# Performance work log

Hardware: AMD Instinct MI355X
Metric: run time of the kernel (lower is better)

The kernel has to match this reference:

```python
import jax, jax.numpy as jnp
import numpy as np

N_NODES = 50000
N_EDGES = 800000
IN_C = 64
OUT_C = 64
HEADS = 4
N_LAYERS = 2
BN_EPS = 1e-5
NEG_SLOPE = 0.2


def setup_inputs() -> dict:
    key = jax.random.key(0)
    ks = jax.random.split(key, 20)
    inp = {
        "x": jax.random.normal(ks[0], (N_NODES, IN_C), dtype=jnp.float32),
        "edge_index": jax.random.randint(ks[1], (2, N_EDGES), 0, N_NODES, dtype=jnp.int64),
        "edge_weight": jax.random.uniform(ks[2], (N_EDGES,), dtype=jnp.float32),
    }
    # per-layer GATConv + BN params (glorot-ish init)
    for i in range(N_LAYERS):
        k = 3 + i * 5
        scale = 1.0 / np.sqrt(IN_C)
        inp[f"W{i}"] = jax.random.normal(ks[k], (IN_C, HEADS * OUT_C), dtype=jnp.float32) * scale
        inp[f"asrc{i}"] = jax.random.normal(ks[k + 1], (HEADS, OUT_C), dtype=jnp.float32) * scale
        inp[f"adst{i}"] = jax.random.normal(ks[k + 2], (HEADS, OUT_C), dtype=jnp.float32) * scale
        inp[f"b{i}"] = jnp.zeros((OUT_C,), dtype=jnp.float32)
        inp[f"gamma{i}"] = jnp.ones((OUT_C,), dtype=jnp.float32)
        inp[f"beta{i}"] = jnp.zeros((OUT_C,), dtype=jnp.float32)
    return inp


def _gat_layer(x, src, dst, W, a_src, a_dst, b):
    # x: [N, C_in]; src/dst: [E'] (with self loops). Per-head dim = OUT_C.
    xh = (x @ W).reshape(-1, HEADS, OUT_C)          # [N, H, C]
    al_src = jnp.sum(xh * a_src[None], axis=-1)      # [N, H]
    al_dst = jnp.sum(xh * a_dst[None], axis=-1)      # [N, H]
    e = jax.nn.leaky_relu(al_src[src] + al_dst[dst], NEG_SLOPE)  # [E', H]
    # segment softmax over edges sharing a destination node
    m = jax.lax.stop_gradient(jax.ops.segment_max(e, dst, num_segments=N_NODES))
    p = jnp.exp(e - m[dst])
    denom = jax.ops.segment_sum(p, dst, num_segments=N_NODES)
    alpha = p / (denom[dst] + 1e-16)                 # [E', H]
    out = jax.ops.segment_sum(alpha[:, :, None] * xh[src], dst, num_segments=N_NODES)  # [N,H,C]
    return out.mean(axis=1) + b                      # concat=False -> mean over heads


def _batchnorm(x, gamma, beta):
    mu = x.mean(axis=0)
    var = x.var(axis=0)
    return gamma * (x - mu) * jax.lax.rsqrt(var + BN_EPS) + beta


def reference(x, edge_index, edge_weight, W0, asrc0, adst0, b0, gamma0, beta0,
              W1, asrc1, adst1, b1, gamma1, beta1):
    # edge_weight is passed as edge_attr to PyG GATConv but edge_dim=None -> ignored.
    loop = jnp.arange(N_NODES, dtype=edge_index.dtype)
    src = jnp.concatenate([edge_index[0], loop])  # add_self_loops=True (PyG default)
    dst = jnp.concatenate([edge_index[1], loop])
    params = [(W0, asrc0, adst0, b0, gamma0, beta0),
              (W1, asrc1, adst1, b1, gamma1, beta1)]
    saved = None
    for (W, a_s, a_d, b, g, bt) in params:
        x = _gat_layer(x, src, dst, W, a_s, a_d, b)
        saved = x
        x = _batchnorm(x, g, bt)
        x = jax.nn.relu(x)
        # dropout(0.5) is identity in eval mode
    return (x, saved)
```

## Files before the change

kernel.cpp:

```cpp
#include <hip/hip_runtime.h>
#include <stdint.h>

#define NEG_SLOPE 0.2f
#define BN_EPS 1e-5f

typedef __attribute__((ext_vector_type(8))) short bf16x8;
typedef __attribute__((ext_vector_type(4))) float f32x4;

__device__ __forceinline__ float bf2f(unsigned short u) {
  union { unsigned int i; float f; } v; v.i = ((unsigned int)u) << 16; return v.f;
}
__device__ __forceinline__ float asf(unsigned int u) {
  union { unsigned int i; float f; } v; v.i = u; return v.f;
}
__device__ __forceinline__ unsigned short f2bf(float f) {
  union { float f; unsigned int i; } v; v.f = f;
  unsigned int i = v.i;
  return (unsigned short)((i + 0x7fffu + ((i >> 16) & 1u)) >> 16);
}
__device__ __forceinline__ float loadF(const void* p, long long i, int f32) {
  return f32 ? ((const float*)p)[i] : bf2f(((const unsigned short*)p)[i]);
}
__device__ __forceinline__ int edge_at(const void* ei, long long idx, int is64) {
  return is64 ? (int)((const long long*)ei)[idx] : ((const int*)ei)[idx];
}

__global__ void detect_kernel(const unsigned short* __restrict__ x,
                              const int* __restrict__ ei32,
                              int* __restrict__ flags) {
  __shared__ int wild, oddnz;
  if (threadIdx.x == 0) { wild = 0; oddnz = 0; }
  __syncthreads();
  int lw = 0, lo = 0;
  for (int i = threadIdx.x; i < 4096; i += 256) {
    unsigned short u = x[i];
    int ex = (u >> 7) & 0xFF;
    if (ex >= 0x86) lw++;
    if (ei32[2 * i + 1] != 0) lo++;
  }
  if (lw) atomicAdd(&wild, lw);
  if (lo) atomicAdd(&oddnz, lo);
  __syncthreads();
  if (threadIdx.x == 0) { flags[0] = (wild > 64) ? 1 : 0; flags[1] = (oddnz == 0) ? 1 : 0; }
}

__global__ __launch_bounds__(256) void wtrans_kernel(
    const void* __restrict__ W0, const void* __restrict__ as0, const void* __restrict__ ad0,
    const void* __restrict__ W1, const void* __restrict__ as1, const void* __restrict__ ad1,
    const int* __restrict__ flags,
    unsigned short* __restrict__ WTx0, unsigned short* __restrict__ WTx1) {
  const void* W = blockIdx.x ? W1 : W0;
  const void* asrc = blockIdx.x ? as1 : as0;
  const void* adst = blockIdx.x ? ad1 : ad0;
  unsigned short* WTx = blockIdx.x ? WTx1 : WTx0;
  int f32 = flags[0];
  __shared__ unsigned short Wl[64 * 258];
  int t = threadIdx.x;
  for (int i = t; i < 64 * 256; i += 256) {
    int k = i >> 8, c = i & 255;
    Wl[k * 258 + c] = f32 ? f2bf(((const float*)W)[i]) : ((const unsigned short*)W)[i];
  }
  __syncthreads();
  {
    int c = t;
    #pragma unroll
    for (int k8 = 0; k8 < 64; k8 += 8) {
      unsigned int p0 = (unsigned int)Wl[(k8 + 0) * 258 + c] | ((unsigned int)Wl[(k8 + 1) * 258 + c] << 16);
      unsigned int p1 = (unsigned int)Wl[(k8 + 2) * 258 + c] | ((unsigned int)Wl[(k8 + 3) * 258 + c] << 16);
      unsigned int p2 = (unsigned int)Wl[(k8 + 4) * 258 + c] | ((unsigned int)Wl[(k8 + 5) * 258 + c] << 16);
      unsigned int p3 = (unsigned int)Wl[(k8 + 6) * 258 + c] | ((unsigned int)Wl[(k8 + 7) * 258 + c] << 16);
      uint4 pk; pk.x = p0; pk.y = p1; pk.z = p2; pk.w = p3;
      *(uint4*)&WTx[c * 64 + k8] = pk;
    }
  }
  for (int idx = t; idx < 512; idx += 256) {
    int r = idx >> 6;
    int k = idx & 63;
    int h = r & 3;
    const void* av = (r >> 2) ? adst : asrc;
    float acc = 0.f;
    #pragma unroll 8
    for (int c = 0; c < 64; c++)
      acc += bf2f(Wl[k * 258 + h * 64 + c]) * loadF(av, h * 64 + c, f32);
    WTx[(256 + r) * 64 + k] = f2bf(acc);
  }
  for (int idx = t; idx < 512; idx += 256) WTx[264 * 64 + idx] = 0;
}

__global__ __launch_bounds__(256) void hist_kernel(const void* __restrict__ ei, int E, int N,
                                                   const int* __restrict__ flags,
                                                   int* __restrict__ deg) {
  int e = blockIdx.x * 256 + threadIdx.x;
  if (e >= E) return;
  int is64 = flags[1];
  int d = edge_at(ei, (long long)E + e, is64);
  d = (d < 0 || d >= N) ? 0 : d;
  atomicAdd(&deg[d], 1);
}

__global__ __launch_bounds__(256) void partial_kernel(const int* __restrict__ deg,
                                                      int* __restrict__ blocksum, int N) {
  int t = threadIdx.x;
  int idx = blockIdx.x * 256 + t;
  int v = (idx < N) ? deg[idx] : 0;
  #pragma unroll
  for (int o = 1; o < 64; o <<= 1) v += __shfl_xor(v, o);
  __shared__ int ws[4];
  if ((t & 63) == 0) ws[t >> 6] = v;
  __syncthreads();
  if (t == 0) blocksum[blockIdx.x] = ws[0] + ws[1] + ws[2] + ws[3];
}

__global__ void scan_base_kernel(const int* __restrict__ blocksum,
                                 int* __restrict__ blockbase, int B) {
  int lane = threadIdx.x;
  int base = 0;
  if (lane == 0) blockbase[0] = 0;
  for (int start = 0; start < B; start += 64) {
    int idx = start + lane;
    int v = (idx < B) ? blocksum[idx] : 0;
    int sc = v;
    #pragma unroll
    for (int o = 1; o < 64; o <<= 1) {
      int u = __shfl_up(sc, o);
      if (lane >= o) sc += u;
    }
    if (idx < B) blockbase[idx + 1] = base + sc;
    base = __shfl(base + sc, 63);
  }
}

__global__ __launch_bounds__(256) void scan_final_kernel(const int* __restrict__ deg,
                                                         const int* __restrict__ blockbase,
                                                         int* __restrict__ offsets, int N) {
  int t = threadIdx.x;
  int lane = t & 63;
  int wid = t >> 6;
  int idx = blockIdx.x * 256 + t;
  int v = (idx < N) ? deg[idx] : 0;
  int sc = v;
  #pragma unroll
  for (int o = 1; o < 64; o <<= 1) {
    int u = __shfl_up(sc, o);
    if (lane >= o) sc += u;
  }
  __shared__ int ws[4];
  if (lane == 63) ws[wid] = sc;
  __syncthreads();
  int add = 0;
  #pragma unroll
  for (int w = 0; w < 4; w++) if (w < wid) add += ws[w];
  if (idx < N) offsets[idx + 1] = blockbase[blockIdx.x] + add + sc;
  if (idx == 0) offsets[0] = 0;
}

__global__ __launch_bounds__(256) void scatter_kernel(
    const void* __restrict__ ei, int E, int N, const int* __restrict__ flags,
    const int* __restrict__ offsets, int* __restrict__ cursor,
    int* __restrict__ csr_src) {
  int e = blockIdx.x * 256 + threadIdx.x;
  if (e >= E) return;
  int is64 = flags[1];
  int s = edge_at(ei, e, is64);
  int d = edge_at(ei, (long long)E + e, is64);
  s = (s < 0 || s >= N) ? 0 : s;
  d = (d < 0 || d >= N) ? 0 : d;
  int pos = offsets[d] + atomicAdd(&cursor[d], 1);
  csr_src[pos] = s;
}

__global__ __launch_bounds__(256, 3) void gemm_mfma(
    const void* __restrict__ x, const unsigned short* __restrict__ WTx,
    const int* __restrict__ flags, int mode,
    const float* __restrict__ gsum, const float* __restrict__ gsq,
    const void* __restrict__ gamma, const void* __restrict__ beta,
    unsigned short* __restrict__ xh, float* __restrict__ als, float* __restrict__ ald,
    int N) {
  __shared__ unsigned short WTs[272 * 68];
  __shared__ unsigned short RP[4][16 * 68];
  __shared__ float bnsc[64], bnsh[64];
  int f32 = flags[0];
  int t = threadIdx.x;
  for (int i = t; i < 272 * 8; i += 256) {
    int c = i >> 3, g = i & 7;
    uint4 v = ((const uint4*)WTx)[i];
    *(uint4*)&WTs[c * 68 + g * 8] = v;
  }
  if (mode == 1 && t < 64) {
    float mu = gsum[t] / (float)N;
    float var = fmaxf(gsq[t] / (float)N - mu * mu, 0.f);
    float sc = loadF(gamma, t, f32) * rsqrtf(var + BN_EPS);
    bnsc[t] = sc;
    bnsh[t] = loadF(beta, t, f32) - mu * sc;
  }
  __syncthreads();

  int wave = t >> 6, lane = t & 63;
  int q = lane >> 4, r16 = lane & 15;
  int m0 = blockIdx.x * 64 + wave * 16;
  if (m0 >= N) return;
  int row = m0 + r16;
  int rowc = row < N ? row : N - 1;

  bf16x8 a0, a1;
  if (mode == 1) {
    const float* xp = (const float*)x + (size_t)rowc * 64 + q * 8;
    float va[8], vb[8];
    *(float4*)&va[0] = ((const float4*)xp)[0];
    *(float4*)&va[4] = ((const float4*)xp)[1];
    *(float4*)&vb[0] = ((const float4*)(xp + 32))[0];
    *(float4*)&vb[4] = ((const float4*)(xp + 32))[1];
    int k0 = q * 8;
    #pragma unroll
    for (int jj = 0; jj < 8; jj++) {
      float v = fmaxf(va[jj] * bnsc[k0 + jj] + bnsh[k0 + jj], 0.f);
      float w = fmaxf(vb[jj] * bnsc[k0 + 32 + jj] + bnsh[k0 + 32 + jj], 0.f);
      a0[jj] = (short)f2bf(v);
      a1[jj] = (short)f2bf(w);
    }
  } else if (f32) {
    const float* xp = (const float*)x + (size_t)rowc * 64 + q * 8;
    float va[8], vb[8];
    *(float4*)&va[0] = ((const float4*)xp)[0];
    *(float4*)&va[4] = ((const float4*)xp)[1];
    *(float4*)&vb[0] = ((const float4*)(xp + 32))[0];
    *(float4*)&vb[4] = ((const float4*)(xp + 32))[1];
    #pragma unroll
    for (int jj = 0; jj < 8; jj++) {
      a0[jj] = (short)f2bf(va[jj]);
      a1[jj] = (short)f2bf(vb[jj]);
    }
  } else {
    const unsigned short* xp = (const unsigned short*)x + (size_t)rowc * 64 + q * 8;
    a0 = *(const bf16x8*)xp;
    a1 = *(const bf16x8*)(xp + 32);
  }

  f32x4 acc[17];
  #pragma unroll
  for (int tt = 0; tt < 17; tt++) acc[tt] = (f32x4){0.f, 0.f, 0.f, 0.f};
  #pragma unroll
  for (int tt = 0; tt < 17; tt++) {
    int c = tt * 16 + r16;
    bf16x8 b0 = *(const bf16x8*)&WTs[c * 68 + q * 8];
    bf16x8 b1 = *(const bf16x8*)&WTs[c * 68 + 32 + q * 8];
    acc[tt] = __builtin_amdgcn_mfma_f32_16x16x32_bf16(a0, b0, acc[tt], 0, 0, 0);
    acc[tt] = __builtin_amdgcn_mfma_f32_16x16x32_bf16(a1, b1, acc[tt], 0, 0, 0);
  }

  {
    int obase = m0 + q * 4;
    #pragma unroll
    for (int rr = 0; rr < 4; rr++) {
      int orow = obase + rr;
      if (orow < N) {
        if (r16 < 4) als[orow * 4 + r16] = acc[16][rr];
        else if (r16 < 8) ald[orow * 4 + (r16 - 4)] = acc[16][rr];
      }
    }
  }
  unsigned short* rp = RP[wave];
  #pragma unroll
  for (int g4 = 0; g4 < 4; g4++) {
    #pragma unroll
    for (int tt2 = 0; tt2 < 4; tt2++) {
      int tile = g4 * 4 + tt2;
      #pragma unroll
      for (int rr = 0; rr < 4; rr++)
        rp[(q * 4 + rr) * 68 + tt2 * 16 + r16] = f2bf(acc[tile][rr]);
    }
    #pragma unroll
    for (int i = 0; i < 2; i++) {
      int g = i * 64 + lane;
      int r = g >> 3;
      int grp = g & 7;
      uint4 v = *(const uint4*)&rp[r * 68 + grp * 8];
      int orow = m0 + r;
      if (orow < N) ((uint4*)xh)[(size_t)orow * 32 + g4 * 8 + grp] = v;
    }
  }
}

__global__ __launch_bounds__(256) void agg_kernel(
    const unsigned short* __restrict__ xh,
    const float* __restrict__ als, const float* __restrict__ ald,
    const int* __restrict__ offsets, const int* __restrict__ csr_src,
    const void* __restrict__ bias, const int* __restrict__ flags,
    float* __restrict__ y, int N) {
  int lane = threadIdx.x & 63;
  int wid = threadIdx.x >> 6;
  int n = blockIdx.x * 4 + wid;
  if (n >= N) return;
  int h = lane >> 4;
  const uint2* xv = (const uint2*)xh;
  float ad = ald[n * 4 + h];
  float e = als[n * 4 + h] + ad;
  e = (e > 0.f) ? e : NEG_SLOPE * e;
  float p = __expf(e);
  float dsum = p;
  uint2 xs = xv[(size_t)n * 64 + lane];
  float a0 = p * asf(xs.x << 16), a1 = p * asf(xs.x & 0xffff0000u);
  float a2 = p * asf(xs.y << 16), a3 = p * asf(xs.y & 0xffff0000u);
  int beg = offsets[n], end = offsets[n + 1];
  int j = beg;
  for (; j + 4 <= end; j += 4) {
    int s0 = csr_src[j];
    int s1 = csr_src[j + 1];
    int s2 = csr_src[j + 2];
    int s3 = csr_src[j + 3];
    uint2 v0 = xv[(size_t)s0 * 64 + lane];
    uint2 v1 = xv[(size_t)s1 * 64 + lane];
    uint2 v2 = xv[(size_t)s2 * 64 + lane];
    uint2 v3 = xv[(size_t)s3 * 64 + lane];
    float e0 = als[s0 * 4 + h] + ad;
    float e1 = als[s1 * 4 + h] + ad;
    float e2 = als[s2 * 4 + h] + ad;
    float e3 = als[s3 * 4 + h] + ad;
    e0 = (e0 > 0.f) ? e0 : NEG_SLOPE * e0;
    e1 = (e1 > 0.f) ? e1 : NEG_SLOPE * e1;
    e2 = (e2 > 0.f) ? e2 : NEG_SLOPE * e2;
    e3 = (e3 > 0.f) ? e3 : NEG_SLOPE * e3;
    float p0 = __expf(e0);
    float p1 = __expf(e1);
    float p2 = __expf(e2);
    float p3 = __expf(e3);
    dsum += p0 + p1 + p2 + p3;
    a0 += p0 * asf(v0.x << 16) + p1 * asf(v1.x << 16)
        + p2 * asf(v2.x << 16) + p3 * asf(v3.x << 16);
    a1 += p0 * asf(v0.x & 0xffff0000u) + p1 * asf(v1.x & 0xffff0000u)
        + p2 * asf(v2.x & 0xffff0000u) + p3 * asf(v3.x & 0xffff0000u);
    a2 += p0 * asf(v0.y << 16) + p1 * asf(v1.y << 16)
        + p2 * asf(v2.y << 16) + p3 * asf(v3.y << 16);
    a3 += p0 * asf(v0.y & 0xffff0000u) + p1 * asf(v1.y & 0xffff0000u)
        + p2 * asf(v2.y & 0xffff0000u) + p3 * asf(v3.y & 0xffff0000u);
  }
  for (; j < end; j++) {
    int s0 = csr_src[j];
    uint2 v0 = xv[(size_t)s0 * 64 + lane];
    float e0 = als[s0 * 4 + h] + ad;
    e0 = (e0 > 0.f) ? e0 : NEG_SLOPE * e0;
    float p0 = __expf(e0);
    dsum += p0;
    a0 += p0 * asf(v0.x << 16);
    a1 += p0 * asf(v0.x & 0xffff0000u);
    a2 += p0 * asf(v0.y << 16);
    a3 += p0 * asf(v0.y & 0xffff0000u);
  }
  float inv = 1.0f / dsum;
  a0 *= inv; a1 *= inv; a2 *= inv; a3 *= inv;
  a0 += __shfl_xor(a0, 16); a0 += __shfl_xor(a0, 32);
  a1 += __shfl_xor(a1, 16); a1 += __shfl_xor(a1, 32);
  a2 += __shfl_xor(a2, 16); a2 += __shfl_xor(a2, 32);
  a3 += __shfl_xor(a3, 16); a3 += __shfl_xor(a3, 32);
  if (lane < 16) {
    int f32 = flags[0];
    float4 o;
    o.x = 0.25f * a0 + loadF(bias, 4 * lane + 0, f32);
    o.y = 0.25f * a1 + loadF(bias, 4 * lane + 1, f32);
    o.z = 0.25f * a2 + loadF(bias, 4 * lane + 2, f32);
    o.w = 0.25f * a3 + loadF(bias, 4 * lane + 3, f32);
    ((float4*)(y + (size_t)n * 64))[lane] = o;
  }
}

__global__ __launch_bounds__(256) void stats_kernel(const float* __restrict__ y,
                                                    float* __restrict__ gsum,
                                                    float* __restrict__ gsq, int N) {
  __shared__ float ls[256], lq[256];
  int t = threadIdx.x;
  int c = t & 63;
  int r0 = blockIdx.x * 4 + (t >> 6);
  float s = 0.f, q = 0.f;
  for (int r = r0; r < N; r += gridDim.x * 4) {
    float v = y[(size_t)r * 64 + c];
    s += v; q += v * v;
  }
  ls[t] = s; lq[t] = q;
  __syncthreads();
  if (t < 64) {
    s = ls[t] + ls[t + 64] + ls[t + 128] + ls[t + 192];
    q = lq[t] + lq[t + 64] + lq[t + 128] + lq[t + 192];
    atomicAdd(&gsum[c], s);
    atomicAdd(&gsq[c], q);
  }
}

__global__ __launch_bounds__(256) void bn_kernel(
    const float* __restrict__ y, const float* __restrict__ gsum, const float* __restrict__ gsq,
    const void* __restrict__ gamma, const void* __restrict__ beta,
    const int* __restrict__ flags, float* __restrict__ out_f, int N) {
  int i = blockIdx.x * 256 + threadIdx.x;
  if (i >= N * 16) return;
  int f32 = flags[0];
  int cg = i & 15;
  float4 v = ((const float4*)y)[i];
  float4 s = ((const float4*)gsum)[cg];
  float4 q = ((const float4*)gsq)[cg];
  float inv_n = 1.0f / (float)N;
  float vv[4] = {v.x, v.y, v.z, v.w};
  float ss[4] = {s.x, s.y, s.z, s.w};
  float qq[4] = {q.x, q.y, q.z, q.w};
  float o[4];
  #pragma unroll
  for (int k = 0; k < 4; k++) {
    float g = loadF(gamma, 4 * cg + k, f32);
    float b = loadF(beta, 4 * cg + k, f32);
    float mu = ss[k] * inv_n;
    float var = fmaxf(qq[k] * inv_n - mu * mu, 0.f);
    float r = g * (vv[k] - mu) * rsqrtf(var + BN_EPS) + b;
    o[k] = r > 0.f ? r : 0.f;
  }
  float4 ov; ov.x = o[0]; ov.y = o[1]; ov.z = o[2]; ov.w = o[3];
  ((float4*)out_f)[i] = ov;
}

extern "C" void kernel_launch(void* const* d_in, const int* in_sizes, int n_in,
                              void* d_out, int out_size, void* d_ws, size_t ws_size,
                              hipStream_t stream) {
  const void* x    = d_in[0];
  const void* ei   = d_in[1];
  const void* W0    = d_in[3];
  const void* asrc0 = d_in[4];
  const void* adst0 = d_in[5];
  const void* b0    = d_in[6];
  const void* g0    = d_in[7];
  const void* be0   = d_in[8];
  const void* W1    = d_in[9];
  const void* asrc1 = d_in[10];
  const void* adst1 = d_in[11];
  const void* b1    = d_in[12];
  const void* g1    = d_in[13];
  const void* be1   = d_in[14];

  int N = in_sizes[0] / 64;
  int E = in_sizes[1] / 2;
  int NB = (N + 255) / 256;
  int NG = (N + 63) / 64;
  int NA = (N + 3) / 4;

  char* p = (char*)d_ws;
  auto alloc = [&](size_t bytes) -> char* {
    char* r = p;
    p += (bytes + 255) & ~(size_t)255;
    return r;
  };
  int* flags    = (int*)alloc(256);
  int* deg      = (int*)alloc((size_t)N * 4);
  int* cursor   = (int*)alloc((size_t)N * 4);
  int* offsets  = (int*)alloc((size_t)(N + 1) * 4);
  int* blocksum = (int*)alloc((size_t)NB * 4);
  int* blockbase= (int*)alloc((size_t)(NB + 1) * 4);
  int* csr_src  = (int*)alloc((size_t)E * 4);
  unsigned short* WTx0 = (unsigned short*)alloc(272 * 64 * 2);
  unsigned short* WTx1 = (unsigned short*)alloc(272 * 64 * 2);
  unsigned short* xh = (unsigned short*)alloc((size_t)N * 256 * 2);
  float* als    = (float*)alloc((size_t)N * 4 * 4);
  float* ald    = (float*)alloc((size_t)N * 4 * 4);
  float* y      = (float*)alloc((size_t)N * 64 * 4);
  float* gsum0  = (float*)alloc(256);
  float* gsq0   = (float*)alloc(256);
  float* gsum1  = (float*)alloc(256);
  float* gsq1   = (float*)alloc(256);

  hipMemsetAsync(deg, 0, (size_t)N * 4, stream);
  hipMemsetAsync(cursor, 0, (size_t)N * 4, stream);
  hipMemsetAsync(gsum0, 0, 1024, stream);

  detect_kernel<<<1, 256, 0, stream>>>((const unsigned short*)x, (const int*)ei, flags);
  wtrans_kernel<<<2, 256, 0, stream>>>(W0, asrc0, adst0, W1, asrc1, adst1, flags, WTx0, WTx1);

  hist_kernel<<<(E + 255) / 256, 256, 0, stream>>>(ei, E, N, flags, deg);
  partial_kernel<<<NB, 256, 0, stream>>>(deg, blocksum, N);
  scan_base_kernel<<<1, 64, 0, stream>>>(blocksum, blockbase, NB);
  scan_final_kernel<<<NB, 256, 0, stream>>>(deg, blockbase, offsets, N);
  scatter_kernel<<<(E + 255) / 256, 256, 0, stream>>>(ei, E, N, flags, offsets, cursor, csr_src);

  float* out_x = (float*)d_out;
  float* out_saved = out_x + (size_t)N * 64;

  gemm_mfma<<<NG, 256, 0, stream>>>(x, WTx0, flags, 0, (const float*)nullptr,
                                    (const float*)nullptr, nullptr, nullptr,
                                    xh, als, ald, N);
  agg_kernel<<<NA, 256, 0, stream>>>(xh, als, ald, offsets, csr_src, b0, flags, y, N);
  stats_kernel<<<250, 256, 0, stream>>>(y, gsum0, gsq0, N);
  gemm_mfma<<<NG, 256, 0, stream>>>(y, WTx1, flags, 1, gsum0, gsq0, g0, be0,
                                    xh, als, ald, N);
  agg_kernel<<<NA, 256, 0, stream>>>(xh, als, ald, offsets, csr_src, b1, flags, out_saved, N);
  stats_kernel<<<250, 256, 0, stream>>>(out_saved, gsum1, gsq1, N);
  bn_kernel<<<(N * 16 + 255) / 256, 256, 0, stream>>>(out_saved, gsum1, gsq1, g1, be1,
                                                      flags, out_x, N);
}
```

Baseline: 428.5 us.

## Use 16-byte gathers with two edges per wave in aggregation; double GEMM rows per block

The aggregation kernel now has each half-wave handle a different edge, with every lane loading 16 bytes (8 bf16) instead of 8. This doubles the edges in flight per wave and widens the memory transactions, at the cost of extra cross-half shuffle reductions and more registers. The projection GEMM kernel now processes two 64-row chunks per block, so the weight staging into shared memory is amortized over twice as many rows and half as many blocks are launched.

```diff
diff --git a/kernel.cpp b/kernel.cpp
--- a/kernel.cpp
+++ b/kernel.cpp
@@ -197,86 +197,90 @@
 
   int wave = t >> 6, lane = t & 63;
   int q = lane >> 4, r16 = lane & 15;
-  int m0 = blockIdx.x * 64 + wave * 16;
-  if (m0 >= N) return;
-  int row = m0 + r16;
-  int rowc = row < N ? row : N - 1;
-
-  bf16x8 a0, a1;
-  if (mode == 1) {
-    const float* xp = (const float*)x + (size_t)rowc * 64 + q * 8;
-    float va[8], vb[8];
-    *(float4*)&va[0] = ((const float4*)xp)[0];
-    *(float4*)&va[4] = ((const float4*)xp)[1];
-    *(float4*)&vb[0] = ((const float4*)(xp + 32))[0];
-    *(float4*)&vb[4] = ((const float4*)(xp + 32))[1];
-    int k0 = q * 8;
+  unsigned short* rp = RP[wave];
+
+  #pragma unroll
+  for (int rb = 0; rb < 2; rb++) {
+    int m0 = blockIdx.x * 128 + rb * 64 + wave * 16;
+    if (m0 >= N) break;
+    int row = m0 + r16;
+    int rowc = row < N ? row : N - 1;
+
+    bf16x8 a0, a1;
+    if (mode == 1) {
+      const float* xp = (const float*)x + (size_t)rowc * 64 + q * 8;
+      float va[8], vb[8];
+      *(float4*)&va[0] = ((const float4*)xp)[0];
+      *(float4*)&va[4] = ((const float4*)xp)[1];
+      *(float4*)&vb[0] = ((const float4*)(xp + 32))[0];
+      *(float4*)&vb[4] = ((const float4*)(xp + 32))[1];
+      int k0 = q * 8;
+      #pragma unroll
+      for (int jj = 0; jj < 8; jj++) {
+        float v = fmaxf(va[jj] * bnsc[k0 + jj] + bnsh[k0 + jj], 0.f);
+        float w = fmaxf(vb[jj] * bnsc[k0 + 32 + jj] + bnsh[k0 + 32 + jj], 0.f);
+        a0[jj] = (short)f2bf(v);
+        a1[jj] = (short)f2bf(w);
+      }
+    } else if (f32) {
+      const float* xp = (const float*)x + (size_t)rowc * 64 + q * 8;
+      float va[8], vb[8];
+      *(float4*)&va[0] = ((const float4*)xp)[0];
+      *(float4*)&va[4] = ((const float4*)xp)[1];
+      *(float4*)&vb[0] = ((const float4*)(xp + 32))[0];
+      *(float4*)&vb[4] = ((const float4*)(xp + 32))[1];
+      #pragma unroll
+      for (int jj = 0; jj < 8; jj++) {
+        a0[jj] = (short)f2bf(va[jj]);
+        a1[jj] = (short)f2bf(vb[jj]);
+      }
+    } else {
+      const unsigned short* xp = (const unsigned short*)x + (size_t)rowc * 64 + q * 8;
+      a0 = *(const bf16x8*)xp;
+      a1 = *(const bf16x8*)(xp + 32);
+    }
+
+    f32x4 acc[17];
     #pragma unroll
-    for (int jj = 0; jj < 8; jj++) {
-      float v = fmaxf(va[jj] * bnsc[k0 + jj] + bnsh[k0 + jj], 0.f);
-      float w = fmaxf(vb[jj] * bnsc[k0 + 32 + jj] + bnsh[k0 + 32 + jj], 0.f);
-      a0[jj] = (short)f2bf(v);
-      a1[jj] = (short)f2bf(w);
-    }
-  } else if (f32) {
-    const float* xp = (const float*)x + (size_t)rowc * 64 + q * 8;
-    float va[8], vb[8];
-    *(float4*)&va[0] = ((const float4*)xp)[0];
-    *(float4*)&va[4] = ((const float4*)xp)[1];
-    *(float4*)&vb[0] = ((const float4*)(xp + 32))[0];
-    *(float4*)&vb[4] = ((const float4*)(xp + 32))[1];
+    for (int tt = 0; tt < 17; tt++) acc[tt] = (f32x4){0.f, 0.f, 0.f, 0.f};
     #pragma unroll
-    for (int jj = 0; jj < 8; jj++) {
-      a0[jj] = (short)f2bf(va[jj]);
-      a1[jj] = (short)f2bf(vb[jj]);
-    }
-  } else {
-    const unsigned short* xp = (const unsigned short*)x + (size_t)rowc * 64 + q * 8;
-    a0 = *(const bf16x8*)xp;
-    a1 = *(const bf16x8*)(xp + 32);
-  }
-
-  f32x4 acc[17];
-  #pragma unroll
-  for (int tt = 0; tt < 17; tt++) acc[tt] = (f32x4){0.f, 0.f, 0.f, 0.f};
-  #pragma unroll
-  for (int tt = 0; tt < 17; tt++) {
-    int c = tt * 16 + r16;
-    bf16x8 b0 = *(const bf16x8*)&WTs[c * 68 + q * 8];
-    bf16x8 b1 = *(const bf16x8*)&WTs[c * 68 + 32 + q * 8];
-    acc[tt] = __builtin_amdgcn_mfma_f32_16x16x32_bf16(a0, b0, acc[tt], 0, 0, 0);
-    acc[tt] = __builtin_amdgcn_mfma_f32_16x16x32_bf16(a1, b1, acc[tt], 0, 0, 0);
-  }
-
-  {
-    int obase = m0 + q * 4;
+    for (int tt = 0; tt < 17; tt++) {
+      int c = tt * 16 + r16;
+      bf16x8 b0 = *(const bf16x8*)&WTs[c * 68 + q * 8];
+      bf16x8 b1 = *(const bf16x8*)&WTs[c * 68 + 32 + q * 8];
+      acc[tt] = __builtin_amdgcn_mfma_f32_16x16x32_bf16(a0, b0, acc[tt], 0, 0, 0);
+      acc[tt] = __builtin_amdgcn_mfma_f32_16x16x32_bf16(a1, b1, acc[tt], 0, 0, 0);
+    }
+
+    {
+      int obase = m0 + q * 4;
+      #pragma unroll
+      for (int rr = 0; rr < 4; rr++) {
+        int orow = obase + rr;
+        if (orow < N) {
+          if (r16 < 4) als[orow * 4 + r16] = acc[16][rr];
+          else if (r16 < 8) ald[orow * 4 + (r16 - 4)] = acc[16][rr];
+        }
+      }
+    }
     #pragma unroll
-    for (int rr = 0; rr < 4; rr++) {
-      int orow = obase + rr;
-      if (orow < N) {
-        if (r16 < 4) als[orow * 4 + r16] = acc[16][rr];
-        else if (r16 < 8) ald[orow * 4 + (r16 - 4)] = acc[16][rr];
+    for (int g4 = 0; g4 < 4; g4++) {
+      #pragma unroll
+      for (int tt2 = 0; tt2 < 4; tt2++) {
+        int tile = g4 * 4 + tt2;
+        #pragma unroll
+        for (int rr = 0; rr < 4; rr++)
+          rp[(q * 4 + rr) * 68 + tt2 * 16 + r16] = f2bf(acc[tile][rr]);
       }
-    }
-  }
-  unsigned short* rp = RP[wave];
-  #pragma unroll
-  for (int g4 = 0; g4 < 4; g4++) {
-    #pragma unroll
-    for (int tt2 = 0; tt2 < 4; tt2++) {
-      int tile = g4 * 4 + tt2;
       #pragma unroll
-      for (int rr = 0; rr < 4; rr++)
-        rp[(q * 4 + rr) * 68 + tt2 * 16 + r16] = f2bf(acc[tile][rr]);
-    }
-    #pragma unroll
-    for (int i = 0; i < 2; i++) {
-      int g = i * 64 + lane;
-      int r = g >> 3;
-      int grp = g & 7;
-      uint4 v = *(const uint4*)&rp[r * 68 + grp * 8];
-      int orow = m0 + r;
-      if (orow < N) ((uint4*)xh)[(size_t)orow * 32 + g4 * 8 + grp] = v;
+      for (int i = 0; i < 2; i++) {
+        int g = i * 64 + lane;
+        int r = g >> 3;
+        int grp = g & 7;
+        uint4 v = *(const uint4*)&rp[r * 68 + grp * 8];
+        int orow = m0 + r;
+        if (orow < N) ((uint4*)xh)[(size_t)orow * 32 + g4 * 8 + grp] = v;
+      }
     }
   }
 }
@@ -291,27 +295,36 @@
   int wid = threadIdx.x >> 6;
   int n = blockIdx.x * 4 + wid;
   if (n >= N) return;
-  int h = lane >> 4;
-  const uint2* xv = (const uint2*)xh;
+  int half = lane >> 5;
+  int hl = lane & 31;
+  int h = hl >> 3;
+  const uint4* xv = (const uint4*)xh;
   float ad = ald[n * 4 + h];
-  float e = als[n * 4 + h] + ad;
-  e = (e > 0.f) ? e : NEG_SLOPE * e;
-  float p = __expf(e);
-  float dsum = p;
-  uint2 xs = xv[(size_t)n * 64 + lane];
-  float a0 = p * asf(xs.x << 16), a1 = p * asf(xs.x & 0xffff0000u);
-  float a2 = p * asf(xs.y << 16), a3 = p * asf(xs.y & 0xffff0000u);
+  float acc0 = 0.f, acc1 = 0.f, acc2 = 0.f, acc3 = 0.f;
+  float acc4 = 0.f, acc5 = 0.f, acc6 = 0.f, acc7 = 0.f;
+  float dsum = 0.f;
+  if (half == 0) {
+    float e = als[n * 4 + h] + ad;
+    e = (e > 0.f) ? e : NEG_SLOPE * e;
+    float p = __expf(e);
+    dsum = p;
+    uint4 v = xv[(size_t)n * 32 + hl];
+    acc0 = p * asf(v.x << 16); acc1 = p * asf(v.x & 0xffff0000u);
+    acc2 = p * asf(v.y << 16); acc3 = p * asf(v.y & 0xffff0000u);
+    acc4 = p * asf(v.z << 16); acc5 = p * asf(v.z & 0xffff0000u);
+    acc6 = p * asf(v.w << 16); acc7 = p * asf(v.w & 0xffff0000u);
+  }
   int beg = offsets[n], end = offsets[n + 1];
   int j = beg;
-  for (; j + 4 <= end; j += 4) {
-    int s0 = csr_src[j];
-    int s1 = csr_src[j + 1];
-    int s2 = csr_src[j + 2];
-    int s3 = csr_src[j + 3];
-    uint2 v0 = xv[(size_t)s0 * 64 + lane];
-    uint2 v1 = xv[(size_t)s1 * 64 + lane];
-    uint2 v2 = xv[(size_t)s2 * 64 + lane];
-    uint2 v3 = xv[(size_t)s3 * 64 + lane];
+  for (; j + 8 <= end; j += 8) {
+    int s0 = csr_src[j + 0 + half];
+    int s1 = csr_src[j + 2 + half];
+    int s2 = csr_src[j + 4 + half];
+    int s3 = csr_src[j + 6 + half];
+    uint4 v0 = xv[(size_t)s0 * 32 + hl];
+    uint4 v1 = xv[(size_t)s1 * 32 + hl];
+    uint4 v2 = xv[(size_t)s2 * 32 + hl];
+    uint4 v3 = xv[(size_t)s3 * 32 + hl];
     float e0 = als[s0 * 4 + h] + ad;
     float e1 = als[s1 * 4 + h] + ad;
     float e2 = als[s2 * 4 + h] + ad;
@@ -325,41 +338,68 @@
     float p2 = __expf(e2);
     float p3 = __expf(e3);
     dsum += p0 + p1 + p2 + p3;
-    a0 += p0 * asf(v0.x << 16) + p1 * asf(v1.x << 16)
-        + p2 * asf(v2.x << 16) + p3 * asf(v3.x << 16);
-    a1 += p0 * asf(v0.x & 0xffff0000u) + p1 * asf(v1.x & 0xffff0000u)
-        + p2 * asf(v2.x & 0xffff0000u) + p3 * asf(v3.x & 0xffff0000u);
-    a2 += p0 * asf(v0.y << 16) + p1 * asf(v1.y << 16)
-        + p2 * asf(v2.y << 16) + p3 * asf(v3.y << 16);
-    a3 += p0 * asf(v0.y & 0xffff0000u) + p1 * asf(v1.y & 0xffff0000u)
-        + p2 * asf(v2.y & 0xffff0000u) + p3 * asf(v3.y & 0xffff0000u);
-  }
-  for (; j < end; j++) {
-    int s0 = csr_src[j];
-    uint2 v0 = xv[(size_t)s0 * 64 + lane];
-    float e0 = als[s0 * 4 + h] + ad;
-    e0 = (e0 > 0.f) ? e0 : NEG_SLOPE * e0;
-    float p0 = __expf(e0);
-    dsum += p0;
-    a0 += p0 * asf(v0.x << 16);
-    a1 += p0 * asf(v0.x & 0xffff0000u);
-    a2 += p0 * asf(v0.y << 16);
-    a3 += p0 * asf(v0.y & 0xffff0000u);
-  }
+    acc0 += p0 * asf(v0.x << 16) + p1 * asf(v1.x << 16)
+          + p2 * asf(v2.x << 16) + p3 * asf(v3.x << 16);
+    acc1 += p0 * asf(v0.x & 0xffff0000u) + p1 * asf(v1.x & 0xffff0000u)
+          + p2 * asf(v2.x & 0xffff0000u) + p3 * asf(v3.x & 0xffff0000u);
+    acc2 += p0 * asf(v0.y << 16) + p1 * asf(v1.y << 16)
+          + p2 * asf(v2.y << 16) + p3 * asf(v3.y << 16);
+    acc3 += p0 * asf(v0.y & 0xffff0000u) + p1 * asf(v1.y & 0xffff0000u)
+          + p2 * asf(v2.y & 0xffff0000u) + p3 * asf(v3.y & 0xffff0000u);
+    acc4 += p0 * asf(v0.z << 16) + p1 * asf(v1.z << 16)
+          + p2 * asf(v2.z << 16) + p3 * asf(v3.z << 16);
+    acc5 += p0 * asf(v0.z & 0xffff0000u) + p1 * asf(v1.z & 0xffff0000u)
+          + p2 * asf(v2.z & 0xffff0000u) + p3 * asf(v3.z & 0xffff0000u);
+    acc6 += p0 * asf(v0.w << 16) + p1 * asf(v1.w << 16)
+          + p2 * asf(v2.w << 16) + p3 * asf(v3.w << 16);
+    acc7 += p0 * asf(v0.w & 0xffff0000u) + p1 * asf(v1.w & 0xffff0000u)
+          + p2 * asf(v2.w & 0xffff0000u) + p3 * asf(v3.w & 0xffff0000u);
+  }
+  for (; j < end; j += 2) {
+    int jj = j + half;
+    if (jj < end) {
+      int s = csr_src[jj];
+      uint4 v = xv[(size_t)s * 32 + hl];
+      float e = als[s * 4 + h] + ad;
+      e = (e > 0.f) ? e : NEG_SLOPE * e;
+      float p = __expf(e);
+      dsum += p;
+      acc0 += p * asf(v.x << 16); acc1 += p * asf(v.x & 0xffff0000u);
+      acc2 += p * asf(v.y << 16); acc3 += p * asf(v.y & 0xffff0000u);
+      acc4 += p * asf(v.z << 16); acc5 += p * asf(v.z & 0xffff0000u);
+      acc6 += p * asf(v.w << 16); acc7 += p * asf(v.w & 0xffff0000u);
+    }
+  }
+  dsum += __shfl_xor(dsum, 32);
+  acc0 += __shfl_xor(acc0, 32); acc1 += __shfl_xor(acc1, 32);
+  acc2 += __shfl_xor(acc2, 32); acc3 += __shfl_xor(acc3, 32);
+  acc4 += __shfl_xor(acc4, 32); acc5 += __shfl_xor(acc5, 32);
+  acc6 += __shfl_xor(acc6, 32); acc7 += __shfl_xor(acc7, 32);
   float inv = 1.0f / dsum;
-  a0 *= inv; a1 *= inv; a2 *= inv; a3 *= inv;
-  a0 += __shfl_xor(a0, 16); a0 += __shfl_xor(a0, 32);
-  a1 += __shfl_xor(a1, 16); a1 += __shfl_xor(a1, 32);
-  a2 += __shfl_xor(a2, 16); a2 += __shfl_xor(a2, 32);
-  a3 += __shfl_xor(a3, 16); a3 += __shfl_xor(a3, 32);
-  if (lane < 16) {
+  acc0 *= inv; acc1 *= inv; acc2 *= inv; acc3 *= inv;
+  acc4 *= inv; acc5 *= inv; acc6 *= inv; acc7 *= inv;
+  acc0 += __shfl_xor(acc0, 8); acc0 += __shfl_xor(acc0, 16);
+  acc1 += __shfl_xor(acc1, 8); acc1 += __shfl_xor(acc1, 16);
+  acc2 += __shfl_xor(acc2, 8); acc2 += __shfl_xor(acc2, 16);
+  acc3 += __shfl_xor(acc3, 8); acc3 += __shfl_xor(acc3, 16);
+  acc4 += __shfl_xor(acc4, 8); acc4 += __shfl_xor(acc4, 16);
+  acc5 += __shfl_xor(acc5, 8); acc5 += __shfl_xor(acc5, 16);
+  acc6 += __shfl_xor(acc6, 8); acc6 += __shfl_xor(acc6, 16);
+  acc7 += __shfl_xor(acc7, 8); acc7 += __shfl_xor(acc7, 16);
+  if (lane < 8) {
     int f32 = flags[0];
-    float4 o;
-    o.x = 0.25f * a0 + loadF(bias, 4 * lane + 0, f32);
-    o.y = 0.25f * a1 + loadF(bias, 4 * lane + 1, f32);
-    o.z = 0.25f * a2 + loadF(bias, 4 * lane + 2, f32);
-    o.w = 0.25f * a3 + loadF(bias, 4 * lane + 3, f32);
-    ((float4*)(y + (size_t)n * 64))[lane] = o;
+    int cb = 8 * lane;
+    float4 o0, o1;
+    o0.x = 0.25f * acc0 + loadF(bias, cb + 0, f32);
+    o0.y = 0.25f * acc1 + loadF(bias, cb + 1, f32);
+    o0.z = 0.25f * acc2 + loadF(bias, cb + 2, f32);
+    o0.w = 0.25f * acc3 + loadF(bias, cb + 3, f32);
+    o1.x = 0.25f * acc4 + loadF(bias, cb + 4, f32);
+    o1.y = 0.25f * acc5 + loadF(bias, cb + 5, f32);
+    o1.z = 0.25f * acc6 + loadF(bias, cb + 6, f32);
+    o1.w = 0.25f * acc7 + loadF(bias, cb + 7, f32);
+    *(float4*)(y + (size_t)n * 64 + cb) = o0;
+    *(float4*)(y + (size_t)n * 64 + cb + 4) = o1;
   }
 }
 
@@ -435,7 +475,7 @@
   int N = in_sizes[0] / 64;
   int E = in_sizes[1] / 2;
   int NB = (N + 255) / 256;
-  int NG = (N + 63) / 64;
+  int NG = (N + 127) / 128;
   int NA = (N + 3) / 4;
 
   char* p = (char*)d_ws;
```

Result: faster. 419.4 us (-2.1%).
